# Optimization experiments

Measured on AMD Instinct MI355X. Metric: run time of the kernel, lower is better.

## Reference

```python
import jax, jax.numpy as jnp
import numpy as np

J = 6                      # KB kernel width (tkbn default numpoints)
ALPHA = 2.34 * J           # tkbn default kbwidth * numpoints
I0A = float(np.i0(ALPHA))


def _apod(N, G):
    """Image-domain apodization: 1 / FT(Kaiser-Bessel kernel), centered length-N."""
    n = jnp.arange(N) - N // 2
    u = n.astype(jnp.float32) / G  # cycles per oversampled-grid sample
    arg = ALPHA ** 2 - (np.pi * J * u) ** 2
    s = jnp.sqrt(jnp.abs(arg) + 1e-20)
    F = jnp.where(arg > 0, jnp.sinh(s) / s, jnp.sin(s) / s) * (J / I0A)
    return 1.0 / F


def _kb_weights(g, G):
    """Separable KB interpolation weights + wrapped grid indices for coords g [K]."""
    base = jnp.floor(g).astype(jnp.int32)
    j = jnp.arange(J, dtype=jnp.int32)
    pts = base[:, None] - (J // 2) + 1 + j            # [K, J] unwrapped grid points
    u = g[:, None] - pts.astype(g.dtype)               # distance in grid units
    x = jnp.maximum(1.0 - (2.0 * u / J) ** 2, 0.0)
    w = jnp.i0(ALPHA * jnp.sqrt(x)) / I0A              # [K, J] real weights
    idx = jnp.mod(pts, G)                              # wrapped indices
    return w.astype(jnp.complex64), idx


def _nufft2(image, kspace):
    """Type-2 NUFFT (image -> nonuniform kspace), KB gridding, ortho norm."""
    H, W = image.shape[-2], image.shape[-1]
    G1, G2 = 2 * H, 2 * W
    img = image[0, 0].astype(jnp.complex64)
    img = img * (_apod(H, G1)[:, None] * _apod(W, G2)[None, :]).astype(jnp.complex64)
    # centered zero-pad to oversampled grid, DC to index 0, FFT (ortho)
    r0, c0 = (G1 - H) // 2, (G2 - W) // 2
    grid = jnp.zeros((G1, G2), jnp.complex64).at[r0:r0 + H, c0:c0 + W].set(img)
    grid = jnp.fft.fft2(jnp.fft.ifftshift(grid)) / np.sqrt(G1 * G2)
    # interpolate at nonuniform frequencies (omega in rad/sample -> grid coords)
    g1 = jnp.mod(kspace[0] * G1 / (2.0 * np.pi), G1)
    g2 = jnp.mod(kspace[1] * G2 / (2.0 * np.pi), G2)
    wx, ix = _kb_weights(g1, G1)
    wy, iy = _kb_weights(g2, G2)
    flat = grid.reshape(-1)
    vals = flat[ix[:, :, None] * G2 + iy[:, None, :]]   # [K, J, J] gather (memory-bound)
    return jnp.einsum('kab,ka,kb->k', vals, wx, wy)


def setup_inputs() -> dict:
    key = jax.random.key(0)
    H = W = 512
    n_ang, n_det = 720, 768
    image = jax.random.normal(key, (1, 1, H, W), dtype=jnp.float32)
    # radial (radon) trajectory: per-angle line of n_det frequencies in [-pi, pi)
    theta = np.linspace(0.0, np.pi, n_ang, endpoint=False)
    kr = (np.arange(n_det) - n_det // 2) / n_det * 2.0 * np.pi
    ky = kr[None, :] * np.sin(theta)[:, None]
    kx = kr[None, :] * np.cos(theta)[:, None]
    kspace = jnp.asarray(np.stack([ky.ravel(), kx.ravel()]), dtype=jnp.float32)
    return {"image": image, "kspace": kspace, "n_ang": n_ang, "n_det": n_det}


def reference(image, kspace, n_ang, n_det):
    kdata = _nufft2(image, kspace).reshape(n_ang, n_det)   # '() () (N M) -> N M'
    kdata = jnp.fft.ifftshift(kdata, axes=1)
    kdata = jnp.fft.ifft(kdata, axis=1).real
    kdata = jnp.fft.fftshift(kdata, axes=1)
    return kdata
```

## Files before the change

kernel.cpp:

```cpp
#include <hip/hip_runtime.h>
#include <math.h>

#define PI_F     3.14159265358979f
#define TWOPI_F  6.283185307179586f
#define ALPHA_F  14.04f
#define NK       552960
#define NANG     720
#define NDET     768

__device__ __forceinline__ float2 cadd(float2 a, float2 b) { return make_float2(a.x+b.x, a.y+b.y); }
__device__ __forceinline__ float2 csub(float2 a, float2 b) { return make_float2(a.x-b.x, a.y-b.y); }
__device__ __forceinline__ float2 cmul(float2 a, float2 b) { return make_float2(a.x*b.x-a.y*b.y, a.x*b.y+a.y*b.x); }

__device__ __forceinline__ float i0f(float x) {
    if (x < 3.75f) {
        float t = x * (1.0f / 3.75f);
        float t2 = t * t;
        return 1.0f + t2 * (3.5156229f + t2 * (3.0899424f + t2 * (1.2067492f +
                     t2 * (0.2659732f + t2 * (0.0360768f + t2 * 0.0045813f)))));
    } else {
        float ti = 3.75f / x;
        float p = 0.39894228f + ti * (0.01328592f + ti * (0.00225319f +
                  ti * (-0.00157565f + ti * (0.00916281f + ti * (-0.02057706f +
                  ti * (0.02635537f + ti * (-0.01647633f + ti * 0.00392377f)))))));
        return __expf(x) * rsqrtf(x) * p;
    }
}

__device__ __forceinline__ float apodf(int i, float inv_i0a) {
    float u = ((float)i - 256.0f) * (1.0f / 1024.0f);
    float pj = PI_F * 6.0f * u;
    float arg = ALPHA_F * ALPHA_F - pj * pj;
    float s = sqrtf(arg);
    float F = sinhf(s) / s * (6.0f * inv_i0a);
    return 1.0f / F;
}

__device__ __forceinline__ float2 mul_ipow(float2 v, int k) {
    switch (k & 3) {
        case 0:  return v;
        case 1:  return make_float2(-v.y,  v.x);
        case 2:  return make_float2(-v.x, -v.y);
        default: return make_float2( v.y, -v.x);
    }
}

template<int N, int LOGN, int B, int T>
__device__ __forceinline__ float2* stockham_b(float2* src, float2* dst,
                                              const float2* __restrict__ tw, int tid) {
    constexpr int HALF = N >> 1;
    int log2s = 0;
    for (int n = N; n > 1; n >>= 1, ++log2s) {
        int h = n >> 1;
        int s = 1 << log2s;
        #pragma unroll
        for (int i = tid; i < B * HALF; i += T) {
            int bb = i >> (LOGN - 1);
            int j  = i & (HALF - 1);
            int q = j & (s - 1);
            int p = j >> log2s;
            float2 w = tw[p << log2s];
            float2* S = src + bb * N;
            float2* D = dst + bb * N;
            float2 a  = S[q + (p << log2s)];
            float2 b2 = S[q + ((p + h) << log2s)];
            float2 su = cadd(a, b2);
            float2 di = csub(a, b2);
            D[q + ((2 * p) << log2s)]     = su;
            D[q + ((2 * p + 1) << log2s)] = cmul(di, w);
        }
        __syncthreads();
        float2* t = src; src = dst; dst = t;
    }
    return src;
}

__global__ __launch_bounds__(256) void fft_rows_kernel(const float* __restrict__ img,
                                                       float2* __restrict__ U) {
    __shared__ float2 bA[1024], bB[1024], tw[512];
    int r = blockIdx.x, t = threadIdx.x;
    for (int j = t; j < 512; j += 256) {
        float ang = -TWOPI_F * (float)j * (1.0f / 1024.0f);
        float sn, cs; sincosf(ang, &sn, &cs);
        tw[j] = make_float2(cs, sn);
    }
    float inv_i0a = 1.0f / i0f(ALPHA_F);
    float ar = apodf(r, inv_i0a);
    for (int c = t; c < 512; c += 256)
        bA[c] = make_float2(img[r * 512 + c] * ar * apodf(c, inv_i0a), 0.0f);
    for (int c = t + 512; c < 1024; c += 256)
        bA[c] = make_float2(0.0f, 0.0f);
    __syncthreads();
    float2* res = stockham_b<1024, 10, 1, 256>(bA, bB, tw, t);
    for (int k = t; k < 1024; k += 256)
        U[r * 1024 + k] = mul_ipow(res[k], k);
}

__global__ __launch_bounds__(512) void fft_cols_kernel(const float2* __restrict__ U,
                                                       float2* __restrict__ GT) {
    __shared__ float2 bA[4096], bB[4096], tw[512];
    int c0 = blockIdx.x * 4, t = threadIdx.x;
    if (t < 512) {
        float ang = -TWOPI_F * (float)t * (1.0f / 1024.0f);
        float sn, cs; sincosf(ang, &sn, &cs);
        tw[t] = make_float2(cs, sn);
    }
    #pragma unroll
    for (int it = 0; it < 4; ++it) {
        int i = t + it * 512;
        int rr = i >> 2, cc = i & 3;
        bA[cc * 1024 + rr] = U[rr * 1024 + c0 + cc];
    }
    #pragma unroll
    for (int it = 0; it < 4; ++it) {
        int i = t + it * 512;
        bA[(i >> 9) * 1024 + 512 + (i & 511)] = make_float2(0.0f, 0.0f);
    }
    __syncthreads();
    float2* res = stockham_b<1024, 10, 4, 512>(bA, bB, tw, t);
    const float sc = 1.0f / 1024.0f;
    #pragma unroll
    for (int it = 0; it < 8; ++it) {
        int i = t + it * 512;
        int cc = i >> 10, k1 = i & 1023;
        float2 v = mul_ipow(res[cc * 1024 + k1], k1);
        GT[(c0 + cc) * 1024 + k1] = make_float2(v.x * sc, v.y * sc);
    }
}

__global__ __launch_bounds__(768) void gather_ifft_kernel(const float* __restrict__ ksp,
                                                          const float2* __restrict__ GT,
                                                          float* __restrict__ out) {
    __shared__ float2 fA[768], fB[768], tw[128];
    __shared__ float tab[1026];
    int t = threadIdx.x;
    int a = (blockIdx.x & 7) * 90 + (blockIdx.x >> 3);
    const float inv_i0a = 1.0f / i0f(ALPHA_F);
    if (t < 128) {
        float ang = TWOPI_F * (float)t * (1.0f / 256.0f);
        float sn, cs; sincosf(ang, &sn, &cs);
        tw[t] = make_float2(cs, sn);
    }
    for (int j = t; j < 1026; j += 768) {
        float u = (float)j * (3.0f / 1024.0f);
        float x = fmaxf(1.0f - (u * u) * (1.0f / 9.0f), 0.0f);
        tab[j] = i0f(ALPHA_F * sqrtf(x)) * inv_i0a;
    }
    __syncthreads();

    int lane = t & 63, wid = t >> 6;
    int l = lane & 3, dsub = lane >> 2;
    float m0 = (float)(2 * l), m1 = (float)(2 * l + 1);

    #pragma unroll
    for (int pass = 0; pass < 4; ++pass) {
        int det = pass * 192 + wid * 16 + dsub;
        int kk = a * NDET + det;
        float ky = ksp[kk];
        float kx = ksp[NK + kk];

        float v1 = ky * (512.0f / PI_F);
        float q1 = v1 * (1.0f / 1024.0f);
        v1 = (q1 - floorf(q1)) * 1024.0f;
        int b1 = (int)floorf(v1);
        int e  = (b1 - 2) & ~1;
        float fe = v1 - (float)e;
        int col8 = ((e + 2 * l) & 1023) * 8;

        float ua = fabsf(fe - m0), ub = fabsf(fe - m1);
        float w1a, w1b;
        {
            float uu = fminf(ua, 3.0f) * (1024.0f / 3.0f);
            int jj = (int)uu; float ff = uu - (float)jj;
            float w = tab[jj] + ff * (tab[jj + 1] - tab[jj]);
            w1a = (ua < 3.0f) ? w : 0.0f;
        }
        {
            float uu = fminf(ub, 3.0f) * (1024.0f / 3.0f);
            int jj = (int)uu; float ff = uu - (float)jj;
            float w = tab[jj] + ff * (tab[jj + 1] - tab[jj]);
            w1b = (ub < 3.0f) ? w : 0.0f;
        }

        float v2 = kx * (512.0f / PI_F);
        float q2 = v2 * (1.0f / 1024.0f);
        v2 = (q2 - floorf(q2)) * 1024.0f;
        int b2 = (int)floorf(v2);
        float frac2 = v2 - (float)b2;

        float accx = 0.0f, accy = 0.0f;
        #pragma unroll
        for (int b = 0; b < 6; ++b) {
            int row = (b2 - 2 + b + 1024) & 1023;
            float u2 = fabsf(frac2 + (float)(2 - b)) * (1024.0f / 3.0f);
            int j2 = (int)u2; float f2 = u2 - (float)j2;
            float w2 = tab[j2] + f2 * (tab[j2 + 1] - tab[j2]);
            float4 f = *(const float4*)((const char*)GT + row * 8192 + col8);
            accx += w2 * (w1a * f.x + w1b * f.z);
            accy += w2 * (w1a * f.y + w1b * f.w);
        }

        accx += __shfl_xor(accx, 1);
        accx += __shfl_xor(accx, 2);
        accy += __shfl_xor(accy, 1);
        accy += __shfl_xor(accy, 2);

        if (l == 0) {
            float sgn = (det & 1) ? -1.0f : 1.0f;
            fA[(det % 3) * 256 + (det / 3)] = make_float2(accx * sgn, accy * sgn);
        }
    }
    __syncthreads();

    float2* F = stockham_b<256, 8, 3, 768>(fA, fB, tw, t);

    int n = t;
    int p = n & 255;
    float2 F0 = F[p], F1 = F[256 + p], F2 = F[512 + p];
    float a1 = TWOPI_F * (float)n * (1.0f / 768.0f);
    float s1, c1, s2, c2;
    __sincosf(a1, &s1, &c1);
    __sincosf(2.0f * a1, &s2, &c2);
    float re = F0.x + (F1.x * c1 - F1.y * s1) + (F2.x * c2 - F2.y * s2);
    float scale = ((n & 1) ? -1.0f : 1.0f) * (1.0f / 768.0f);
    out[a * NDET + n] = re * scale;
}

extern "C" void kernel_launch(void* const* d_in, const int* in_sizes, int n_in,
                              void* d_out, int out_size, void* d_ws, size_t ws_size,
                              hipStream_t stream) {
    (void)in_sizes; (void)n_in; (void)out_size; (void)ws_size;
    const float* image = (const float*)d_in[0];
    const float* ksp   = (const float*)d_in[1];

    float2* U  = (float2*)d_ws;
    float2* GT = U + 512 * 1024;
    float*  outp = (float*)d_out;

    hipLaunchKernelGGL(fft_rows_kernel,    dim3(512), dim3(256), 0, stream, image, U);
    hipLaunchKernelGGL(fft_cols_kernel,    dim3(256), dim3(512), 0, stream, U, GT);
    hipLaunchKernelGGL(gather_ifft_kernel, dim3(NANG), dim3(768), 0, stream, ksp, GT, outp);
}
```

Measured before the change: 103.2 us.

## Exploit real-input Hermitian symmetry in 2D FFT and pack KB table with slopes

The row FFT now packs two real image rows into one complex FFT and separates them with conjugate-symmetric unpacking, halving the row-FFT block count. The column FFT computes only about half of the columns and fills the rest of the grid through Hermitian symmetry, so each block writes conjugate-mirrored output. The Kaiser-Bessel lookup table stores value and slope pairs, so each interpolation needs one LDS read and an FMA. The cost is extra scattered mirrored global writes and a reliance on the input being real.

```diff
diff --git a/kernel.cpp b/kernel.cpp
--- a/kernel.cpp
+++ b/kernel.cpp
@@ -25,6 +25,11 @@
                   ti * (0.02635537f + ti * (-0.01647633f + ti * 0.00392377f)))))));
         return __expf(x) * rsqrtf(x) * p;
     }
+}
+
+__device__ __forceinline__ float kbw(float u, float inv_i0a) {
+    float x = fmaxf(1.0f - (u * u) * (1.0f / 9.0f), 0.0f);
+    return i0f(ALPHA_F * sqrtf(x)) * inv_i0a;
 }
 
 __device__ __forceinline__ float apodf(int i, float inv_i0a) {
@@ -78,22 +83,32 @@
 __global__ __launch_bounds__(256) void fft_rows_kernel(const float* __restrict__ img,
                                                        float2* __restrict__ U) {
     __shared__ float2 bA[1024], bB[1024], tw[512];
-    int r = blockIdx.x, t = threadIdx.x;
+    int r0 = blockIdx.x * 2, t = threadIdx.x;
     for (int j = t; j < 512; j += 256) {
         float ang = -TWOPI_F * (float)j * (1.0f / 1024.0f);
         float sn, cs; sincosf(ang, &sn, &cs);
         tw[j] = make_float2(cs, sn);
     }
     float inv_i0a = 1.0f / i0f(ALPHA_F);
-    float ar = apodf(r, inv_i0a);
-    for (int c = t; c < 512; c += 256)
-        bA[c] = make_float2(img[r * 512 + c] * ar * apodf(c, inv_i0a), 0.0f);
+    float ar0 = apodf(r0, inv_i0a);
+    float ar1 = apodf(r0 + 1, inv_i0a);
+    for (int c = t; c < 512; c += 256) {
+        float ac = apodf(c, inv_i0a);
+        bA[c] = make_float2(img[r0 * 512 + c] * ar0 * ac,
+                            img[(r0 + 1) * 512 + c] * ar1 * ac);
+    }
     for (int c = t + 512; c < 1024; c += 256)
         bA[c] = make_float2(0.0f, 0.0f);
     __syncthreads();
     float2* res = stockham_b<1024, 10, 1, 256>(bA, bB, tw, t);
-    for (int k = t; k < 1024; k += 256)
-        U[r * 1024 + k] = mul_ipow(res[k], k);
+    for (int k = t; k < 1024; k += 256) {
+        float2 X0 = res[k];
+        float2 Xm = res[(1024 - k) & 1023];
+        float2 A0 = make_float2(0.5f * (X0.x + Xm.x), 0.5f * (X0.y - Xm.y));
+        float2 A1 = make_float2(0.5f * (X0.y + Xm.y), -0.5f * (X0.x - Xm.x));
+        U[r0 * 1024 + k]       = mul_ipow(A0, k);
+        U[(r0 + 1) * 1024 + k] = mul_ipow(A1, k);
+    }
 }
 
 __global__ __launch_bounds__(512) void fft_cols_kernel(const float2* __restrict__ U,
@@ -123,8 +138,12 @@
     for (int it = 0; it < 8; ++it) {
         int i = t + it * 512;
         int cc = i >> 10, k1 = i & 1023;
+        int ccg = c0 + cc;
         float2 v = mul_ipow(res[cc * 1024 + k1], k1);
-        GT[(c0 + cc) * 1024 + k1] = make_float2(v.x * sc, v.y * sc);
+        v = make_float2(v.x * sc, v.y * sc);
+        GT[ccg * 1024 + k1] = v;
+        if (ccg >= 1 && ccg <= 508)
+            GT[(1024 - ccg) * 1024 + ((1024 - k1) & 1023)] = make_float2(v.x, -v.y);
     }
 }
 
@@ -132,7 +151,7 @@
                                                           const float2* __restrict__ GT,
                                                           float* __restrict__ out) {
     __shared__ float2 fA[768], fB[768], tw[128];
-    __shared__ float tab[1026];
+    __shared__ float2 tab2[1026];
     int t = threadIdx.x;
     int a = (blockIdx.x & 7) * 90 + (blockIdx.x >> 3);
     const float inv_i0a = 1.0f / i0f(ALPHA_F);
@@ -142,9 +161,9 @@
         tw[t] = make_float2(cs, sn);
     }
     for (int j = t; j < 1026; j += 768) {
-        float u = (float)j * (3.0f / 1024.0f);
-        float x = fmaxf(1.0f - (u * u) * (1.0f / 9.0f), 0.0f);
-        tab[j] = i0f(ALPHA_F * sqrtf(x)) * inv_i0a;
+        float w0 = kbw((float)j * (3.0f / 1024.0f), inv_i0a);
+        float w1 = kbw((float)(j + 1) * (3.0f / 1024.0f), inv_i0a);
+        tab2[j] = make_float2(w0, w1 - w0);
     }
     __syncthreads();
 
@@ -172,14 +191,14 @@
         {
             float uu = fminf(ua, 3.0f) * (1024.0f / 3.0f);
             int jj = (int)uu; float ff = uu - (float)jj;
-            float w = tab[jj] + ff * (tab[jj + 1] - tab[jj]);
-            w1a = (ua < 3.0f) ? w : 0.0f;
+            float2 td = tab2[jj];
+            w1a = (ua < 3.0f) ? fmaf(ff, td.y, td.x) : 0.0f;
         }
         {
             float uu = fminf(ub, 3.0f) * (1024.0f / 3.0f);
             int jj = (int)uu; float ff = uu - (float)jj;
-            float w = tab[jj] + ff * (tab[jj + 1] - tab[jj]);
-            w1b = (ub < 3.0f) ? w : 0.0f;
+            float2 td = tab2[jj];
+            w1b = (ub < 3.0f) ? fmaf(ff, td.y, td.x) : 0.0f;
         }
 
         float v2 = kx * (512.0f / PI_F);
@@ -194,7 +213,8 @@
             int row = (b2 - 2 + b + 1024) & 1023;
             float u2 = fabsf(frac2 + (float)(2 - b)) * (1024.0f / 3.0f);
             int j2 = (int)u2; float f2 = u2 - (float)j2;
-            float w2 = tab[j2] + f2 * (tab[j2 + 1] - tab[j2]);
+            float2 td = tab2[j2];
+            float w2 = fmaf(f2, td.y, td.x);
             float4 f = *(const float4*)((const char*)GT + row * 8192 + col8);
             accx += w2 * (w1a * f.x + w1b * f.z);
             accy += w2 * (w1a * f.y + w1b * f.w);
@@ -237,7 +257,7 @@
     float2* GT = U + 512 * 1024;
     float*  outp = (float*)d_out;
 
-    hipLaunchKernelGGL(fft_rows_kernel,    dim3(512), dim3(256), 0, stream, image, U);
-    hipLaunchKernelGGL(fft_cols_kernel,    dim3(256), dim3(512), 0, stream, U, GT);
+    hipLaunchKernelGGL(fft_rows_kernel,    dim3(256), dim3(256), 0, stream, image, U);
+    hipLaunchKernelGGL(fft_cols_kernel,    dim3(129), dim3(512), 0, stream, U, GT);
     hipLaunchKernelGGL(gather_ifft_kernel, dim3(NANG), dim3(768), 0, stream, ksp, GT, outp);
 }
```

Result: faster. 95.28 us (-7.7%).
